# Kernel tuning notes

Hardware: AMD Instinct MI355X
Metric: run time of the kernel (lower is better)

Reference implementation:

```python
import jax, jax.numpy as jnp
import numpy as np

N_A = 100000
N_B = 100000
D = 128
E = 400000


def setup_inputs() -> dict:
    key = jax.random.key(0)
    ks = jax.random.split(key, 14)
    inp = {
        'x_A': jax.random.normal(ks[0], (N_A, D), dtype=jnp.float32),
        'x_B': jax.random.normal(ks[1], (N_B, D), dtype=jnp.float32),
        'W_msg_ab1': jax.random.normal(ks[2], (D, D), dtype=jnp.float32) / np.sqrt(D),
        'W_self_ab1': jax.random.normal(ks[3], (D, D), dtype=jnp.float32) / np.sqrt(D),
        'W_msg_ab2': jax.random.normal(ks[4], (D, D), dtype=jnp.float32) / np.sqrt(D),
        'W_self_ab2': jax.random.normal(ks[5], (D, D), dtype=jnp.float32) / np.sqrt(D),
        'W_msg_ba': jax.random.normal(ks[6], (D, D), dtype=jnp.float32) / np.sqrt(D),
        'W_self_ba': jax.random.normal(ks[7], (D, D), dtype=jnp.float32) / np.sqrt(D),
        'src_ab1': jax.random.randint(ks[8], (E,), 0, N_A, dtype=jnp.int32),
        'dst_ab1': jax.random.randint(ks[9], (E,), 0, N_B, dtype=jnp.int32),
        'src_ab2': jax.random.randint(ks[10], (E,), 0, N_A, dtype=jnp.int32),
        'dst_ab2': jax.random.randint(ks[11], (E,), 0, N_B, dtype=jnp.int32),
        'src_ba': jax.random.randint(ks[12], (E,), 0, N_B, dtype=jnp.int32),
        'dst_ba': jax.random.randint(ks[13], (E,), 0, N_A, dtype=jnp.int32),
    }
    return inp


def _conv(x_src, x_dst, src_idx, dst_idx, num_dst, W_msg, W_self):
    # gather -> transform -> scatter-add, plus dst self-transform
    msg = x_src[src_idx] @ W_msg                              # [E, D]
    agg = jax.ops.segment_sum(msg, dst_idx, num_segments=num_dst)  # [num_dst, D]
    return agg + x_dst @ W_self


def reference(x_A, x_B,
              W_msg_ab1, W_self_ab1, W_msg_ab2, W_self_ab2,
              W_msg_ba, W_self_ba,
              src_ab1, dst_ab1, src_ab2, dst_ab2, src_ba, dst_ba):
    # two edge types with dst_type B are accumulated (out_dict[dst] + result)
    out_B = _conv(x_A, x_B, src_ab1, dst_ab1, N_B, W_msg_ab1, W_self_ab1) \
          + _conv(x_A, x_B, src_ab2, dst_ab2, N_B, W_msg_ab2, W_self_ab2)
    out_A = _conv(x_B, x_A, src_ba, dst_ba, N_A, W_msg_ba, W_self_ba)
    return out_A, out_B
```

## Files before the change

### kernel.cpp

```cpp
#include <hip/hip_runtime.h>

constexpr int D   = 128;
constexpr int NA  = 100000;
constexpr int NB  = 100000;
constexpr int NE  = 400000;
constexpr int CAP = 24;

typedef __attribute__((ext_vector_type(8))) short           bf16x8;
typedef __attribute__((ext_vector_type(4))) float           f32x4;
typedef __attribute__((ext_vector_type(4))) unsigned short  us4;

static __device__ __forceinline__ unsigned short f2bf(float f) {
    unsigned u = __float_as_uint(f);
    unsigned r = (u + 0x7FFFu + ((u >> 16) & 1u)) >> 16;
    return (unsigned short)r;
}

__global__ __launch_bounds__(256) void prep_weights_kernel(
    unsigned short* __restrict__ WT,
    const float* __restrict__ Wmba,  const float* __restrict__ Wsba,
    const float* __restrict__ Wmab1, const float* __restrict__ Wmab2,
    const float* __restrict__ Wsab1, const float* __restrict__ Wsab2)
{
    int idx = blockIdx.x * 256 + threadIdx.x;
    int m   = idx >> 14;
    int rem = idx & 16383;
    int c   = rem >> 7;
    int k   = rem & 127;
    float v;
    if      (m == 0) v = Wmba [k * D + c];
    else if (m == 1) v = Wsba [k * D + c];
    else if (m == 2) v = Wmab1[k * D + c];
    else if (m == 3) v = Wmab2[k * D + c];
    else             v = Wsab1[k * D + c] + Wsab2[k * D + c];
    WT[idx] = f2bf(v);
}

__global__ __launch_bounds__(256) void fill_kernel(
    int* __restrict__ cursor, int* __restrict__ slots,
    const int* __restrict__ src, const int* __restrict__ dst, int E)
{
    int e = blockIdx.x * 256 + threadIdx.x;
    if (e >= E) return;
    int d = dst[e];
    int pos = atomicAdd(&cursor[d], 1);
    if (pos < CAP) slots[(size_t)d * CAP + pos] = src[e];
}

template<int NBF>
__global__ __launch_bounds__(256) void fused_gnn_kernel(
    float* __restrict__ out,
    const float* __restrict__ XM,
    const int* __restrict__ cur0, const int* __restrict__ sl0,
    const int* __restrict__ cur1, const int* __restrict__ sl1,
    const float* __restrict__ XS,
    const unsigned short* __restrict__ WT0,
    const unsigned short* __restrict__ WT1,
    const unsigned short* __restrict__ WTS,
    int N)
{
    __shared__ unsigned short tile[NBF][64][128];

    const int tid  = threadIdx.x;
    const int row0 = blockIdx.x * 64;

    {
        const int lj   = tid & 31;
        const int rsub = tid >> 5;
        #pragma unroll
        for (int p = 0; p < NBF; ++p) {
            const int* __restrict__ cur = (p == 0) ? cur0 : cur1;
            const int* __restrict__ sl  = (p == 0) ? sl0  : sl1;
            #pragma unroll
            for (int it = 0; it < 8; ++it) {
                int rl = it * 8 + rsub;
                int r  = row0 + rl;
                float4 a0 = make_float4(0.f, 0.f, 0.f, 0.f);
                float4 a1 = make_float4(0.f, 0.f, 0.f, 0.f);
                if (r < N) {
                    int deg = min(cur[r], CAP);
                    const int* s = sl + (size_t)r * CAP;
                    int i = 0;
                    for (; i + 1 < deg; i += 2) {
                        int s0 = s[i], s1 = s[i + 1];
                        float4 v0 = *reinterpret_cast<const float4*>(XM + (size_t)s0 * D + lj * 4);
                        float4 v1 = *reinterpret_cast<const float4*>(XM + (size_t)s1 * D + lj * 4);
                        a0.x += v0.x; a0.y += v0.y; a0.z += v0.z; a0.w += v0.w;
                        a1.x += v1.x; a1.y += v1.y; a1.z += v1.z; a1.w += v1.w;
                    }
                    if (i < deg) {
                        float4 v0 = *reinterpret_cast<const float4*>(XM + (size_t)s[i] * D + lj * 4);
                        a0.x += v0.x; a0.y += v0.y; a0.z += v0.z; a0.w += v0.w;
                    }
                    a0.x += a1.x; a0.y += a1.y; a0.z += a1.z; a0.w += a1.w;
                }
                us4 o;
                o.x = f2bf(a0.x); o.y = f2bf(a0.y); o.z = f2bf(a0.z); o.w = f2bf(a0.w);
                int cb = (lj * 8) ^ ((rl & 7) << 4);
                *reinterpret_cast<us4*>(reinterpret_cast<char*>(&tile[p][rl][0]) + cb) = o;
            }
        }
    }
    __syncthreads();

    const int lane = tid & 63;
    const int wid  = tid >> 6;
    const int g    = lane >> 4;
    const int m    = lane & 15;
    const int rl0  = wid * 16;

    f32x4 acc[8];
    #pragma unroll
    for (int ct = 0; ct < 8; ++ct) acc[ct] = (f32x4){0.f, 0.f, 0.f, 0.f};

    #pragma unroll
    for (int p = 0; p < NBF; ++p) {
        bf16x8 af[4];
        const char* rowp = reinterpret_cast<const char*>(&tile[p][rl0 + m][0]);
        #pragma unroll
        for (int ks = 0; ks < 4; ++ks) {
            int cb = (g * 16 + ks * 64) ^ ((m & 7) << 4);
            af[ks] = *reinterpret_cast<const bf16x8*>(rowp + cb);
        }
        const unsigned short* __restrict__ W = (p == 0) ? WT0 : WT1;
        #pragma unroll
        for (int ct = 0; ct < 8; ++ct) {
            const unsigned short* wp = W + (size_t)(ct * 16 + m) * D + g * 8;
            #pragma unroll
            for (int ks = 0; ks < 4; ++ks) {
                bf16x8 bfv = *reinterpret_cast<const bf16x8*>(wp + ks * 32);
                acc[ct] = __builtin_amdgcn_mfma_f32_16x16x32_bf16(af[ks], bfv, acc[ct], 0, 0, 0);
            }
        }
    }

    {
        int r = row0 + rl0 + m;
        r = (r < N) ? r : (N - 1);
        const float* ap = XS + (size_t)r * D + g * 8;
        bf16x8 af[4];
        #pragma unroll
        for (int ks = 0; ks < 4; ++ks) {
            float4 lo = *reinterpret_cast<const float4*>(ap + ks * 32);
            float4 hi = *reinterpret_cast<const float4*>(ap + ks * 32 + 4);
            bf16x8 f;
            f[0] = (short)f2bf(lo.x); f[1] = (short)f2bf(lo.y);
            f[2] = (short)f2bf(lo.z); f[3] = (short)f2bf(lo.w);
            f[4] = (short)f2bf(hi.x); f[5] = (short)f2bf(hi.y);
            f[6] = (short)f2bf(hi.z); f[7] = (short)f2bf(hi.w);
            af[ks] = f;
        }
        #pragma unroll
        for (int ct = 0; ct < 8; ++ct) {
            const unsigned short* wp = WTS + (size_t)(ct * 16 + m) * D + g * 8;
            #pragma unroll
            for (int ks = 0; ks < 4; ++ks) {
                bf16x8 bfv = *reinterpret_cast<const bf16x8*>(wp + ks * 32);
                acc[ct] = __builtin_amdgcn_mfma_f32_16x16x32_bf16(af[ks], bfv, acc[ct], 0, 0, 0);
            }
        }
    }

    const int r0 = row0 + rl0 + g * 4;
    #pragma unroll
    for (int ct = 0; ct < 8; ++ct) {
        int col = ct * 16 + m;
        #pragma unroll
        for (int j = 0; j < 4; ++j) {
            int r = r0 + j;
            if (r < N) out[(size_t)r * D + col] = acc[ct][j];
        }
    }
}

extern "C" void kernel_launch(void* const* d_in, const int* in_sizes, int n_in,
                              void* d_out, int out_size, void* d_ws, size_t ws_size,
                              hipStream_t stream)
{
    const float* x_A        = (const float*)d_in[0];
    const float* x_B        = (const float*)d_in[1];
    const float* W_msg_ab1  = (const float*)d_in[2];
    const float* W_self_ab1 = (const float*)d_in[3];
    const float* W_msg_ab2  = (const float*)d_in[4];
    const float* W_self_ab2 = (const float*)d_in[5];
    const float* W_msg_ba   = (const float*)d_in[6];
    const float* W_self_ba  = (const float*)d_in[7];
    const int* src_ab1 = (const int*)d_in[8];
    const int* dst_ab1 = (const int*)d_in[9];
    const int* src_ab2 = (const int*)d_in[10];
    const int* dst_ab2 = (const int*)d_in[11];
    const int* src_ba  = (const int*)d_in[12];
    const int* dst_ba  = (const int*)d_in[13];

    float* out_A = (float*)d_out;
    float* out_B = out_A + (size_t)NA * D;

    char* ws = (char*)d_ws;
    int* cur = (int*)ws;
    int* cur0 = cur;
    int* cur1 = cur + NA;
    int* cur2 = cur + 2 * NA;
    int* sl0 = cur + 3 * NA;
    int* sl1 = sl0 + (size_t)NA * CAP;
    int* sl2 = sl1 + (size_t)NA * CAP;
    unsigned short* WT = (unsigned short*)(sl2 + (size_t)NA * CAP);
    unsigned short* WT_mba  = WT;
    unsigned short* WT_sba  = WT + 1 * D * D;
    unsigned short* WT_mab1 = WT + 2 * D * D;
    unsigned short* WT_mab2 = WT + 3 * D * D;
    unsigned short* WT_sab  = WT + 4 * D * D;

    const dim3 blk(256);
    const int fill_blocks = (NE + 255) / 256;
    const int gnn_blocks  = (NA + 63) / 64;

    prep_weights_kernel<<<5 * D * D / 256, blk, 0, stream>>>(
        WT, W_msg_ba, W_self_ba, W_msg_ab1, W_msg_ab2, W_self_ab1, W_self_ab2);

    hipMemsetAsync(cur, 0, 3 * (size_t)NA * sizeof(int), stream);
    fill_kernel<<<fill_blocks, blk, 0, stream>>>(cur0, sl0, src_ba,  dst_ba,  NE);
    fill_kernel<<<fill_blocks, blk, 0, stream>>>(cur1, sl1, src_ab1, dst_ab1, NE);
    fill_kernel<<<fill_blocks, blk, 0, stream>>>(cur2, sl2, src_ab2, dst_ab2, NE);

    fused_gnn_kernel<1><<<gnn_blocks, blk, 0, stream>>>(
        out_A, x_B, cur0, sl0, nullptr, nullptr, x_A, WT_mba, nullptr, WT_sba, NA);

    fused_gnn_kernel<2><<<gnn_blocks, blk, 0, stream>>>(
        out_B, x_A, cur1, sl1, cur2, sl2, x_B, WT_mab1, WT_mab2, WT_sab, NB);
}
```

Measured before the change: 566.4 us.

## Pre-convert features to bf16 and split gather-sum from MFMA GEMM

Node features are converted to bf16 once up front, so neighbor gathers read half the bytes. Aggregation moves out of the fused kernel into a separate gather_sum kernel that writes bf16 aggregates to workspace, and a standalone MFMA GEMM kernel consumes them. The three edge-fill launches are merged into one. In exchange the pipeline gains extra global round trips for the converted features and the aggregate buffers, more kernel launches, and bf16 rounding of inputs before summation.

```diff
diff --git a/kernel.cpp b/kernel.cpp
--- a/kernel.cpp
+++ b/kernel.cpp
@@ -14,6 +14,9 @@
     unsigned u = __float_as_uint(f);
     unsigned r = (u + 0x7FFFu + ((u >> 16) & 1u)) >> 16;
     return (unsigned short)r;
+}
+static __device__ __forceinline__ float bf2f(unsigned short u) {
+    return __uint_as_float((unsigned)u << 16);
 }
 
 __global__ __launch_bounds__(256) void prep_weights_kernel(
@@ -36,93 +39,106 @@
     WT[idx] = f2bf(v);
 }
 
-__global__ __launch_bounds__(256) void fill_kernel(
-    int* __restrict__ cursor, int* __restrict__ slots,
-    const int* __restrict__ src, const int* __restrict__ dst, int E)
-{
-    int e = blockIdx.x * 256 + threadIdx.x;
-    if (e >= E) return;
-    int d = dst[e];
-    int pos = atomicAdd(&cursor[d], 1);
-    if (pos < CAP) slots[(size_t)d * CAP + pos] = src[e];
-}
-
-template<int NBF>
-__global__ __launch_bounds__(256) void fused_gnn_kernel(
+__global__ __launch_bounds__(256) void convert_x_kernel(
+    unsigned short* __restrict__ xb,
+    const float* __restrict__ xA, const float* __restrict__ xB)
+{
+    const size_t half = (size_t)NA * D;
+    size_t i = ((size_t)blockIdx.x * 256 + threadIdx.x) * 8;
+    const float* src = (i < half) ? (xA + i) : (xB + (i - half));
+    float4 lo = *reinterpret_cast<const float4*>(src);
+    float4 hi = *reinterpret_cast<const float4*>(src + 4);
+    bf16x8 o;
+    o[0] = (short)f2bf(lo.x); o[1] = (short)f2bf(lo.y);
+    o[2] = (short)f2bf(lo.z); o[3] = (short)f2bf(lo.w);
+    o[4] = (short)f2bf(hi.x); o[5] = (short)f2bf(hi.y);
+    o[6] = (short)f2bf(hi.z); o[7] = (short)f2bf(hi.w);
+    *reinterpret_cast<bf16x8*>(xb + i) = o;
+}
+
+__global__ __launch_bounds__(256) void fill_all_kernel(
+    int* __restrict__ cur, int* __restrict__ slots,
+    const int* __restrict__ s0, const int* __restrict__ d0,
+    const int* __restrict__ s1, const int* __restrict__ d1,
+    const int* __restrict__ s2, const int* __restrict__ d2)
+{
+    int idx = blockIdx.x * 256 + threadIdx.x;
+    if (idx >= 3 * NE) return;
+    int t = idx / NE;
+    int e = idx - t * NE;
+    const int* sp = (t == 0) ? s0 : (t == 1) ? s1 : s2;
+    const int* dp = (t == 0) ? d0 : (t == 1) ? d1 : d2;
+    int d = dp[e];
+    int pos = atomicAdd(&cur[t * NA + d], 1);
+    if (pos < CAP) slots[((size_t)t * NA + d) * CAP + pos] = sp[e];
+}
+
+__global__ __launch_bounds__(256) void gather_sum_kernel(
+    unsigned short* __restrict__ G, const unsigned short* __restrict__ Xb,
+    const int* __restrict__ cur, const int* __restrict__ slots, int N)
+{
+    int t = blockIdx.x * 256 + threadIdx.x;
+    int r = t >> 4;
+    if (r >= N) return;
+    int j = (t & 15) * 8;
+    int deg = min(cur[r], CAP);
+    const int* sl = slots + (size_t)r * CAP;
+    float a0[8] = {0,0,0,0,0,0,0,0};
+    float a1[8] = {0,0,0,0,0,0,0,0};
+    int i = 0;
+    for (; i + 1 < deg; i += 2) {
+        int s0 = sl[i], s1 = sl[i + 1];
+        bf16x8 v0 = *reinterpret_cast<const bf16x8*>(Xb + (size_t)s0 * D + j);
+        bf16x8 v1 = *reinterpret_cast<const bf16x8*>(Xb + (size_t)s1 * D + j);
+        #pragma unroll
+        for (int k = 0; k < 8; ++k) {
+            a0[k] += bf2f((unsigned short)v0[k]);
+            a1[k] += bf2f((unsigned short)v1[k]);
+        }
+    }
+    if (i < deg) {
+        bf16x8 v0 = *reinterpret_cast<const bf16x8*>(Xb + (size_t)sl[i] * D + j);
+        #pragma unroll
+        for (int k = 0; k < 8; ++k) a0[k] += bf2f((unsigned short)v0[k]);
+    }
+    bf16x8 o;
+    #pragma unroll
+    for (int k = 0; k < 8; ++k) o[k] = (short)f2bf(a0[k] + a1[k]);
+    *reinterpret_cast<bf16x8*>(G + (size_t)r * D + j) = o;
+}
+
+template<int NP>
+__global__ __launch_bounds__(256) void mfma_gemm_kernel(
     float* __restrict__ out,
-    const float* __restrict__ XM,
-    const int* __restrict__ cur0, const int* __restrict__ sl0,
-    const int* __restrict__ cur1, const int* __restrict__ sl1,
-    const float* __restrict__ XS,
-    const unsigned short* __restrict__ WT0,
-    const unsigned short* __restrict__ WT1,
-    const unsigned short* __restrict__ WTS,
+    const unsigned short* __restrict__ A0, const unsigned short* __restrict__ A1,
+    const unsigned short* __restrict__ A2,
+    const unsigned short* __restrict__ W0, const unsigned short* __restrict__ W1,
+    const unsigned short* __restrict__ W2,
     int N)
 {
-    __shared__ unsigned short tile[NBF][64][128];
-
     const int tid  = threadIdx.x;
-    const int row0 = blockIdx.x * 64;
-
-    {
-        const int lj   = tid & 31;
-        const int rsub = tid >> 5;
-        #pragma unroll
-        for (int p = 0; p < NBF; ++p) {
-            const int* __restrict__ cur = (p == 0) ? cur0 : cur1;
-            const int* __restrict__ sl  = (p == 0) ? sl0  : sl1;
-            #pragma unroll
-            for (int it = 0; it < 8; ++it) {
-                int rl = it * 8 + rsub;
-                int r  = row0 + rl;
-                float4 a0 = make_float4(0.f, 0.f, 0.f, 0.f);
-                float4 a1 = make_float4(0.f, 0.f, 0.f, 0.f);
-                if (r < N) {
-                    int deg = min(cur[r], CAP);
-                    const int* s = sl + (size_t)r * CAP;
-                    int i = 0;
-                    for (; i + 1 < deg; i += 2) {
-                        int s0 = s[i], s1 = s[i + 1];
-                        float4 v0 = *reinterpret_cast<const float4*>(XM + (size_t)s0 * D + lj * 4);
-                        float4 v1 = *reinterpret_cast<const float4*>(XM + (size_t)s1 * D + lj * 4);
-                        a0.x += v0.x; a0.y += v0.y; a0.z += v0.z; a0.w += v0.w;
-                        a1.x += v1.x; a1.y += v1.y; a1.z += v1.z; a1.w += v1.w;
-                    }
-                    if (i < deg) {
-                        float4 v0 = *reinterpret_cast<const float4*>(XM + (size_t)s[i] * D + lj * 4);
-                        a0.x += v0.x; a0.y += v0.y; a0.z += v0.z; a0.w += v0.w;
-                    }
-                    a0.x += a1.x; a0.y += a1.y; a0.z += a1.z; a0.w += a1.w;
-                }
-                us4 o;
-                o.x = f2bf(a0.x); o.y = f2bf(a0.y); o.z = f2bf(a0.z); o.w = f2bf(a0.w);
-                int cb = (lj * 8) ^ ((rl & 7) << 4);
-                *reinterpret_cast<us4*>(reinterpret_cast<char*>(&tile[p][rl][0]) + cb) = o;
-            }
-        }
-    }
-    __syncthreads();
-
     const int lane = tid & 63;
     const int wid  = tid >> 6;
     const int g    = lane >> 4;
     const int m    = lane & 15;
-    const int rl0  = wid * 16;
+    const int rbase = blockIdx.x * 64 + wid * 16;
+
+    int r = rbase + m;
+    r = (r < N) ? r : (N - 1);
 
     f32x4 acc[8];
     #pragma unroll
     for (int ct = 0; ct < 8; ++ct) acc[ct] = (f32x4){0.f, 0.f, 0.f, 0.f};
 
     #pragma unroll
-    for (int p = 0; p < NBF; ++p) {
+    for (int p = 0; p < NP; ++p) {
+        const unsigned short* __restrict__ A = (p == 0) ? A0 : (p == 1) ? A1 : A2;
+        const unsigned short* __restrict__ W = (p == 0) ? W0 : (p == 1) ? W1 : W2;
         bf16x8 af[4];
-        const char* rowp = reinterpret_cast<const char*>(&tile[p][rl0 + m][0]);
-        #pragma unroll
-        for (int ks = 0; ks < 4; ++ks) {
-            int cb = (g * 16 + ks * 64) ^ ((m & 7) << 4);
-            af[ks] = *reinterpret_cast<const bf16x8*>(rowp + cb);
-        }
-        const unsigned short* __restrict__ W = (p == 0) ? WT0 : WT1;
+        const unsigned short* ap = A + (size_t)r * D + g * 8;
+        #pragma unroll
+        for (int ks = 0; ks < 4; ++ks)
+            af[ks] = *reinterpret_cast<const bf16x8*>(ap + ks * 32);
         #pragma unroll
         for (int ct = 0; ct < 8; ++ct) {
             const unsigned short* wp = W + (size_t)(ct * 16 + m) * D + g * 8;
@@ -134,41 +150,14 @@
         }
     }
 
-    {
-        int r = row0 + rl0 + m;
-        r = (r < N) ? r : (N - 1);
-        const float* ap = XS + (size_t)r * D + g * 8;
-        bf16x8 af[4];
-        #pragma unroll
-        for (int ks = 0; ks < 4; ++ks) {
-            float4 lo = *reinterpret_cast<const float4*>(ap + ks * 32);
-            float4 hi = *reinterpret_cast<const float4*>(ap + ks * 32 + 4);
-            bf16x8 f;
-            f[0] = (short)f2bf(lo.x); f[1] = (short)f2bf(lo.y);
-            f[2] = (short)f2bf(lo.z); f[3] = (short)f2bf(lo.w);
-            f[4] = (short)f2bf(hi.x); f[5] = (short)f2bf(hi.y);
-            f[6] = (short)f2bf(hi.z); f[7] = (short)f2bf(hi.w);
-            af[ks] = f;
-        }
-        #pragma unroll
-        for (int ct = 0; ct < 8; ++ct) {
-            const unsigned short* wp = WTS + (size_t)(ct * 16 + m) * D + g * 8;
-            #pragma unroll
-            for (int ks = 0; ks < 4; ++ks) {
-                bf16x8 bfv = *reinterpret_cast<const bf16x8*>(wp + ks * 32);
-                acc[ct] = __builtin_amdgcn_mfma_f32_16x16x32_bf16(af[ks], bfv, acc[ct], 0, 0, 0);
-            }
-        }
-    }
-
-    const int r0 = row0 + rl0 + g * 4;
+    const int r0 = rbase + g * 4;
     #pragma unroll
     for (int ct = 0; ct < 8; ++ct) {
         int col = ct * 16 + m;
         #pragma unroll
         for (int j = 0; j < 4; ++j) {
-            int r = r0 + j;
-            if (r < N) out[(size_t)r * D + col] = acc[ct][j];
+            int rr = r0 + j;
+            if (rr < N) out[(size_t)rr * D + col] = acc[ct][j];
         }
     }
 }
@@ -196,14 +185,14 @@
     float* out_B = out_A + (size_t)NA * D;
 
     char* ws = (char*)d_ws;
-    int* cur = (int*)ws;
-    int* cur0 = cur;
-    int* cur1 = cur + NA;
-    int* cur2 = cur + 2 * NA;
-    int* sl0 = cur + 3 * NA;
-    int* sl1 = sl0 + (size_t)NA * CAP;
-    int* sl2 = sl1 + (size_t)NA * CAP;
-    unsigned short* WT = (unsigned short*)(sl2 + (size_t)NA * CAP);
+    unsigned short* xb  = (unsigned short*)ws;
+    unsigned short* xbA = xb;
+    unsigned short* xbB = xb + (size_t)NA * D;
+    unsigned short* G0  = xbB + (size_t)NB * D;
+    unsigned short* G1  = G0 + (size_t)NA * D;
+    int* cur   = (int*)(G1 + (size_t)NA * D);
+    int* slots = cur + 3 * NA;
+    unsigned short* WT = (unsigned short*)(slots + (size_t)3 * NA * CAP);
     unsigned short* WT_mba  = WT;
     unsigned short* WT_sba  = WT + 1 * D * D;
     unsigned short* WT_mab1 = WT + 2 * D * D;
@@ -211,20 +200,26 @@
     unsigned short* WT_sab  = WT + 4 * D * D;
 
     const dim3 blk(256);
-    const int fill_blocks = (NE + 255) / 256;
-    const int gnn_blocks  = (NA + 63) / 64;
+    const int cv_blocks   = (2 * NA * D / 8) / 256;
+    const int fa_blocks   = (3 * NE + 255) / 256;
+    const int gs_blocks   = (NA * 16) / 256;
+    const int gm_blocks   = (NA + 63) / 64;
 
     prep_weights_kernel<<<5 * D * D / 256, blk, 0, stream>>>(
         WT, W_msg_ba, W_self_ba, W_msg_ab1, W_msg_ab2, W_self_ab1, W_self_ab2);
-
+    convert_x_kernel<<<cv_blocks, blk, 0, stream>>>(xb, x_A, x_B);
     hipMemsetAsync(cur, 0, 3 * (size_t)NA * sizeof(int), stream);
-    fill_kernel<<<fill_blocks, blk, 0, stream>>>(cur0, sl0, src_ba,  dst_ba,  NE);
-    fill_kernel<<<fill_blocks, blk, 0, stream>>>(cur1, sl1, src_ab1, dst_ab1, NE);
-    fill_kernel<<<fill_blocks, blk, 0, stream>>>(cur2, sl2, src_ab2, dst_ab2, NE);
-
-    fused_gnn_kernel<1><<<gnn_blocks, blk, 0, stream>>>(
-        out_A, x_B, cur0, sl0, nullptr, nullptr, x_A, WT_mba, nullptr, WT_sba, NA);
-
-    fused_gnn_kernel<2><<<gnn_blocks, blk, 0, stream>>>(
-        out_B, x_A, cur1, sl1, cur2, sl2, x_B, WT_mab1, WT_mab2, WT_sab, NB);
-}
+    fill_all_kernel<<<fa_blocks, blk, 0, stream>>>(
+        cur, slots, src_ba, dst_ba, src_ab1, dst_ab1, src_ab2, dst_ab2);
+
+    gather_sum_kernel<<<gs_blocks, blk, 0, stream>>>(G0, xbB, cur, slots, NA);
+    mfma_gemm_kernel<2><<<gm_blocks, blk, 0, stream>>>(
+        out_A, G0, xbA, nullptr, WT_mba, WT_sba, nullptr, NA);
+
+    gather_sum_kernel<<<gs_blocks, blk, 0, stream>>>(
+        G0, xbA, cur + NA, slots + (size_t)NA * CAP, NB);
+    gather_sum_kernel<<<gs_blocks, blk, 0, stream>>>(
+        G1, xbA, cur + 2 * NA, slots + (size_t)2 * NA * CAP, NB);
+    mfma_gemm_kernel<3><<<gm_blocks, blk, 0, stream>>>(
+        out_B, G0, G1, xbB, WT_mab1, WT_mab2, WT_sab, NB);
+}
```

After: 504.6 us. -10.9%, faster.
